# Performance work log

Measured on AMD Instinct MI355X. Metric: run time of the kernel, lower is better.

The kernel has to match this reference:

```python
import jax, jax.numpy as jnp
import numpy as np

FEATURE_DIM = 256
TEMP = 0.1
BASE_TEMP = 0.07
MAX_SAMPLES = 1024
SIM_THR = 0.7


def setup_inputs() -> dict:
    key = jax.random.key(0)
    ks = jax.random.split(key, 8)
    B, C, H, W = 4, FEATURE_DIM, 160, 160
    s = 1.0 / np.sqrt(C)
    return {
        'feats': jax.random.normal(ks[0], (B, C, H, W), jnp.float32),
        'labels': jax.random.randint(ks[1], (B, H, W), 0, 2).astype(jnp.int64),
        'superpixel_indice': jax.random.randint(ks[2], (B, H, W), 0, 200).astype(jnp.int64),
        'w1': jax.random.normal(ks[3], (C, C), jnp.float32) * s,
        'b1': jnp.zeros((C,), jnp.float32),
        'w2': jax.random.normal(ks[4], (C, C), jnp.float32) * s,
        'b2': jnp.zeros((C,), jnp.float32),
        'wa1': jax.random.normal(ks[5], (64, C), jnp.float32) * s,
        'ba1': jnp.zeros((64,), jnp.float32),
        'wa2': jax.random.normal(ks[6], (1, 64), jnp.float32) * (1.0 / 8.0),
        'ba2': jnp.zeros((1,), jnp.float32),
    }


def _per_sample(f, w, lab, sp):
    # f: (N, C) normalized proj feats, w: (N,) pixel weights, lab/sp: (N,) int
    valid = lab == 1
    # deterministic sample: stable-sort valid pixels to the front, take MAX_SAMPLES
    order = jnp.argsort(jnp.where(valid, 0, 1).astype(jnp.int32))
    idx = order[:MAX_SAMPLES]
    sel = valid[idx]                       # (S,) real-sample mask (pads if <S valid)
    tf = f[idx]                            # (S, C)
    tw = w[idx]                            # (S,)
    ts = sp[idx]                           # (S,)
    sim = tf @ tf.T                        # (S, S)
    S = MAX_SAMPLES
    eye = jnp.eye(S, dtype=bool)
    pos = (ts[:, None] == ts[None, :]) & (sim > SIM_THR)
    pos = pos & sel[:, None] & sel[None, :] & ~eye
    exp_sim = jnp.exp(sim / TEMP) * sel[None, :].astype(sim.dtype)
    denom = exp_sim.sum(axis=1)            # (S,)
    log_prob = sim / TEMP - jnp.log(jnp.where(denom > 0, denom, 1.0))[:, None]
    pw = tw[:, None] * tw[None, :]
    pwm = jnp.where(pos, pw, 0.0)
    psum = pwm.sum()
    loss = -(TEMP / BASE_TEMP) * (pwm * jnp.where(pos, log_prob, 0.0)).sum() / jnp.where(psum > 0, psum, 1.0)
    has = psum > 0
    return jnp.where(has, loss, 0.0), has


def reference(feats, labels, superpixel_indice, w1, b1, w2, b2, wa1, ba1, wa2, ba2):
    B, C, H, W = feats.shape
    x = jnp.transpose(feats, (0, 2, 3, 1)).reshape(B, H * W, C)  # (B, N, C)
    proj = jax.nn.relu(x @ w1.T + b1) @ w2.T + b2                # 1x1 convs == per-pixel matmul
    attn = jax.nn.sigmoid(jax.nn.relu(x @ wa1.T + ba1) @ wa2.T + ba2)[..., 0]  # (B, N)
    nrm = jnp.linalg.norm(proj, axis=-1, keepdims=True)
    fn = proj / jnp.maximum(nrm, 1e-12)
    lab = labels.reshape(B, -1)
    sp = superpixel_indice.reshape(B, -1)
    losses, flags = jax.vmap(_per_sample)(fn, attn, lab, sp)
    n = flags.sum().astype(jnp.float32)
    return jnp.where(n > 0, losses.sum() / jnp.maximum(n, 1.0), 0.0)
```

## Files before the change

### kernel.cpp

```cpp
#include <hip/hip_runtime.h>
#include <hip/hip_bf16.h>
#include <math.h>

#define NPIX   25600
#define CDIM   256
#define SSEL   1024
#define BATCH  4
#define NCHUNK 25
#define INV_T  10.0f
#define RATIO  1.4285714285714286f
#define THR    0.7f

typedef __attribute__((ext_vector_type(8))) short bf16x8;
typedef __attribute__((ext_vector_type(4))) float f32x4;
typedef unsigned short u16;

__device__ __forceinline__ void bf16_split(float v, u16& h, u16& l) {
  __hip_bfloat16 hb = __float2bfloat16(v);
  __hip_bfloat16 lb = __float2bfloat16(v - __bfloat162float(hb));
  h = *reinterpret_cast<u16*>(&hb);
  l = *reinterpret_cast<u16*>(&lb);
}

__global__ __launch_bounds__(256) void pack_weights(
    const float* __restrict__ w1, const float* __restrict__ w2,
    const float* __restrict__ wa1, const int* __restrict__ labels,
    u16* __restrict__ w1hb, u16* __restrict__ w1lb,
    u16* __restrict__ w2hb, u16* __restrict__ w2lb,
    u16* __restrict__ wahb, u16* __restrict__ walb,
    float* __restrict__ denom, float* __restrict__ Prow, float* __restrict__ Ssum,
    float* __restrict__ nrm, int* __restrict__ counts) {
  int t = threadIdx.x;
  int e = blockIdx.x * 256 + t;
  if (e < 65536) {
    bf16_split(w1[e], w1hb[e], w1lb[e]);
    bf16_split(w2[e], w2hb[e], w2lb[e]);
  }
  if (e < 16384) bf16_split(wa1[e], wahb[e], walb[e]);
  if (e < BATCH * SSEL) { denom[e] = 0.f; Prow[e] = 0.f; nrm[e] = 0.f; }
  if (e < BATCH) Ssum[e] = 0.f;

  if (blockIdx.x < BATCH * NCHUNK) {
    int b = blockIdx.x / NCHUNK, ch = blockIdx.x % NCHUNK;
    const int* lab = labels + b * NPIX + ch * 1024;
    int local = 0;
#pragma unroll
    for (int qq = 0; qq < 4; ++qq) local += (lab[qq * 256 + t] == 1);
    for (int off = 32; off > 0; off >>= 1) local += __shfl_xor(local, off, 64);
    __shared__ int ws[4];
    if ((t & 63) == 0) ws[t >> 6] = local;
    __syncthreads();
    if (t == 0) counts[blockIdx.x] = ws[0] + ws[1] + ws[2] + ws[3];
  }
}

__global__ __launch_bounds__(1024) void select_scatter(
    const int* __restrict__ labels, const int* __restrict__ sp,
    const int* __restrict__ counts,
    int* __restrict__ idx, int* __restrict__ selv, int* __restrict__ tsp) {
  int b = blockIdx.x / NCHUNK, ch = blockIdx.x % NCHUNK;
  int t = threadIdx.x;
  __shared__ int cs[NCHUNK];
  __shared__ int wave_tot[16];
  if (t < NCHUNK) cs[t] = counts[b * NCHUNK + t];
  __syncthreads();
  int Vtot = 0, vbase = 0;
#pragma unroll
  for (int c = 0; c < NCHUNK; ++c) {
    int v = cs[c];
    Vtot += v;
    if (c < ch) vbase += v;
  }
  int ibase = ch * 1024 - vbase;

  int i = ch * 1024 + t;
  int isv = (labels[b * NPIX + i] == 1) ? 1 : 0;
  int lane = t & 63, wid = t >> 6;
  unsigned long long mv = __ballot(isv);
  int pv = __popcll(mv & ((1ull << lane) - 1ull));
  if (lane == 0) wave_tot[wid] = __popcll(mv);
  __syncthreads();
  for (int w = 0; w < wid; ++w) pv += wave_tot[w];
  int gslot = isv ? (vbase + pv) : (Vtot + ibase + (t - pv));
  if (gslot < SSEL) {
    idx [b * SSEL + gslot] = i;
    selv[b * SSEL + gslot] = isv;
    tsp [b * SSEL + gslot] = sp[b * NPIX + i];
  }
}

__global__ __launch_bounds__(256) void gather_cast(
    const float* __restrict__ feats, const int* __restrict__ idx,
    u16* __restrict__ xh, u16* __restrict__ xl) {
  int r0 = blockIdx.x * 16;
  int b  = r0 >> 10;
  int t  = threadIdx.x;
  __shared__ int ridx[16];
  if (t < 16) ridx[t] = idx[r0 + t];
  __syncthreads();
  const float* fb = feats + ((long)b * CDIM + t) * NPIX;
#pragma unroll 4
  for (int r = 0; r < 16; ++r) {
    float v = fb[ridx[r]];
    u16 h, l;
    bf16_split(v, h, l);
    long o = (long)(r0 + r) * CDIM + t;
    xh[o] = h;
    xl[o] = l;
  }
}

__global__ __launch_bounds__(256) void gemm1_kernel(
    const u16* __restrict__ xh, const u16* __restrict__ xl,
    const u16* __restrict__ w1hb, const u16* __restrict__ w1lb,
    const u16* __restrict__ wahb, const u16* __restrict__ walb,
    const float* __restrict__ b1, const float* __restrict__ ba1,
    const float* __restrict__ wa2, const float* __restrict__ ba2,
    u16* __restrict__ hh, u16* __restrict__ hl, float* __restrict__ tw) {
  int n  = blockIdx.x;
  int i0 = blockIdx.y * 64;
  int t = threadIdx.x;
  int lane = t & 63, w = t >> 6, m = lane & 15, q = lane >> 4;
  bool attn = (n == 4);
  const u16* bsh = attn ? wahb : (w1hb + n * 64 * 256);
  const u16* bsl = attn ? walb : (w1lb + n * 64 * 256);

  __shared__ __align__(16) u16 Ah[64 * 72], Al[64 * 72];
  __shared__ __align__(16) u16 Bh[64 * 72], Bl[64 * 72];

  f32x4 acc[4];
#pragma unroll
  for (int nt = 0; nt < 4; ++nt) acc[nt] = {0.f, 0.f, 0.f, 0.f};

  for (int kk = 0; kk < 4; ++kk) {
    __syncthreads();
#pragma unroll
    for (int p = 0; p < 2; ++p) {
      int e = p * 256 + t;
      int row = e >> 3, kg = e & 7;
      int lo = row * 72 + kg * 8;
      int go = row * 256 + kk * 64 + kg * 8;
      *(uint4*)&Ah[lo] = *(const uint4*)&xh[(i0 + row) * 256 + kk * 64 + kg * 8];
      *(uint4*)&Al[lo] = *(const uint4*)&xl[(i0 + row) * 256 + kk * 64 + kg * 8];
      *(uint4*)&Bh[lo] = *(const uint4*)&bsh[go];
      *(uint4*)&Bl[lo] = *(const uint4*)&bsl[go];
    }
    __syncthreads();
#pragma unroll
    for (int ks = 0; ks < 2; ++ks) {
      int koff = ks * 32 + q * 8;
      bf16x8 ah = *(const bf16x8*)&Ah[(w * 16 + m) * 72 + koff];
      bf16x8 al = *(const bf16x8*)&Al[(w * 16 + m) * 72 + koff];
#pragma unroll
      for (int nt = 0; nt < 4; ++nt) {
        bf16x8 bh = *(const bf16x8*)&Bh[(nt * 16 + m) * 72 + koff];
        bf16x8 bl = *(const bf16x8*)&Bl[(nt * 16 + m) * 72 + koff];
        acc[nt] = __builtin_amdgcn_mfma_f32_16x16x32_bf16(ah, bh, acc[nt], 0, 0, 0);
        acc[nt] = __builtin_amdgcn_mfma_f32_16x16x32_bf16(ah, bl, acc[nt], 0, 0, 0);
        acc[nt] = __builtin_amdgcn_mfma_f32_16x16x32_bf16(al, bh, acc[nt], 0, 0, 0);
      }
    }
  }

  if (!attn) {
#pragma unroll
    for (int nt = 0; nt < 4; ++nt) {
      int col = n * 64 + nt * 16 + m;
      float bb = b1[col];
#pragma unroll
      for (int reg = 0; reg < 4; ++reg) {
        int row = i0 + w * 16 + q * 4 + reg;
        float v = fmaxf(acc[nt][reg] + bb, 0.f);
        u16 h, l;
        bf16_split(v, h, l);
        hh[row * 256 + col] = h;
        hl[row * 256 + col] = l;
      }
    }
  } else {
    float part[4] = {0.f, 0.f, 0.f, 0.f};
#pragma unroll
    for (int nt = 0; nt < 4; ++nt) {
      int ca = nt * 16 + m;
      float bb = ba1[ca], wv = wa2[ca];
#pragma unroll
      for (int reg = 0; reg < 4; ++reg)
        part[reg] += fmaxf(acc[nt][reg] + bb, 0.f) * wv;
    }
    for (int off = 8; off > 0; off >>= 1) {
#pragma unroll
      for (int reg = 0; reg < 4; ++reg)
        part[reg] += __shfl_xor(part[reg], off, 64);
    }
    if (m == 0) {
      float bb2 = ba2[0];
#pragma unroll
      for (int reg = 0; reg < 4; ++reg) {
        int row = i0 + w * 16 + q * 4 + reg;
        tw[row] = 1.f / (1.f + expf(-(part[reg] + bb2)));
      }
    }
  }
}

__global__ __launch_bounds__(256) void gemm2_kernel(
    const u16* __restrict__ hh, const u16* __restrict__ hl,
    const u16* __restrict__ w2hb, const u16* __restrict__ w2lb,
    const float* __restrict__ b2,
    float* __restrict__ pbuf, float* __restrict__ nrm) {
  int n  = blockIdx.x;
  int i0 = blockIdx.y * 64;
  int t = threadIdx.x;
  int lane = t & 63, w = t >> 6, m = lane & 15, q = lane >> 4;
  const u16* bsh = w2hb + n * 64 * 256;
  const u16* bsl = w2lb + n * 64 * 256;

  __shared__ __align__(16) u16 Ah[64 * 72], Al[64 * 72];
  __shared__ __align__(16) u16 Bh[64 * 72], Bl[64 * 72];

  f32x4 acc[4];
#pragma unroll
  for (int nt = 0; nt < 4; ++nt) acc[nt] = {0.f, 0.f, 0.f, 0.f};

  for (int kk = 0; kk < 4; ++kk) {
    __syncthreads();
#pragma unroll
    for (int p = 0; p < 2; ++p) {
      int e = p * 256 + t;
      int row = e >> 3, kg = e & 7;
      int lo = row * 72 + kg * 8;
      int go = row * 256 + kk * 64 + kg * 8;
      *(uint4*)&Ah[lo] = *(const uint4*)&hh[(i0 + row) * 256 + kk * 64 + kg * 8];
      *(uint4*)&Al[lo] = *(const uint4*)&hl[(i0 + row) * 256 + kk * 64 + kg * 8];
      *(uint4*)&Bh[lo] = *(const uint4*)&bsh[go];
      *(uint4*)&Bl[lo] = *(const uint4*)&bsl[go];
    }
    __syncthreads();
#pragma unroll
    for (int ks = 0; ks < 2; ++ks) {
      int koff = ks * 32 + q * 8;
      bf16x8 ah = *(const bf16x8*)&Ah[(w * 16 + m) * 72 + koff];
      bf16x8 al = *(const bf16x8*)&Al[(w * 16 + m) * 72 + koff];
#pragma unroll
      for (int nt = 0; nt < 4; ++nt) {
        bf16x8 bh = *(const bf16x8*)&Bh[(nt * 16 + m) * 72 + koff];
        bf16x8 bl = *(const bf16x8*)&Bl[(nt * 16 + m) * 72 + koff];
        acc[nt] = __builtin_amdgcn_mfma_f32_16x16x32_bf16(ah, bh, acc[nt], 0, 0, 0);
        acc[nt] = __builtin_amdgcn_mfma_f32_16x16x32_bf16(ah, bl, acc[nt], 0, 0, 0);
        acc[nt] = __builtin_amdgcn_mfma_f32_16x16x32_bf16(al, bh, acc[nt], 0, 0, 0);
      }
    }
  }

  float part[4] = {0.f, 0.f, 0.f, 0.f};
#pragma unroll
  for (int nt = 0; nt < 4; ++nt) {
    int col = n * 64 + nt * 16 + m;
    float bb = b2[col];
#pragma unroll
    for (int reg = 0; reg < 4; ++reg) {
      int row = i0 + w * 16 + q * 4 + reg;
      float p = acc[nt][reg] + bb;
      pbuf[row * 256 + col] = p;
      part[reg] += p * p;
    }
  }
  for (int off = 8; off > 0; off >>= 1) {
#pragma unroll
    for (int reg = 0; reg < 4; ++reg)
      part[reg] += __shfl_xor(part[reg], off, 64);
  }
  if (m == 0) {
#pragma unroll
    for (int reg = 0; reg < 4; ++reg) {
      int row = i0 + w * 16 + q * 4 + reg;
      atomicAdd(&nrm[row], part[reg]);
    }
  }
}

__global__ __launch_bounds__(256) void norm_split(
    const float* __restrict__ pbuf, const float* __restrict__ nrm,
    u16* __restrict__ fnh, u16* __restrict__ fnl) {
  int e = blockIdx.x * 256 + threadIdx.x;
  long base = (long)e * 8;
  int row = e >> 5;
  float inv = 1.f / fmaxf(sqrtf(nrm[row]), 1e-12f);
  float4 pa = *(const float4*)&pbuf[base];
  float4 pb = *(const float4*)&pbuf[base + 4];
  float v[8] = {pa.x, pa.y, pa.z, pa.w, pb.x, pb.y, pb.z, pb.w};
  u16 hs[8], ls[8];
#pragma unroll
  for (int j = 0; j < 8; ++j) bf16_split(v[j] * inv, hs[j], ls[j]);
  *(uint4*)&fnh[base] = *(const uint4*)hs;
  *(uint4*)&fnl[base] = *(const uint4*)ls;
}

__global__ __launch_bounds__(256) void sim_kernel(
    const u16* __restrict__ fnh, const u16* __restrict__ fnl,
    const float* __restrict__ tw,
    const int* __restrict__ selv, const int* __restrict__ tsp,
    float* __restrict__ denom, float* __restrict__ Prow, float* __restrict__ Ssum) {
  int b = blockIdx.y;
  int t = threadIdx.x;
  int lane = t & 63, w = t >> 6;
  int m = lane & 15, q = lane >> 4;

  int rem = blockIdx.x, ti = 0;
  while (rem >= (16 - ti)) { rem -= (16 - ti); ++ti; }
  int tj = ti + rem;
  bool diag = (ti == tj);
  int i0 = ti * 64, j0 = tj * 64;
  int base = b << 10;

  __shared__ __align__(16) u16 Ah[64 * 72], Al[64 * 72];
  __shared__ __align__(16) u16 Bhh[64 * 72], Bll[64 * 72];
  __shared__ float drl[64], Prl[64];
  __shared__ float dclw[4][64], Pclw[4][64];
  __shared__ float swv[4];

  const u16* Bh = diag ? Ah : Bhh;
  const u16* Bl = diag ? Al : Bll;

  f32x4 acc[4];
#pragma unroll
  for (int nt = 0; nt < 4; ++nt) acc[nt] = {0.f, 0.f, 0.f, 0.f};

  for (int kk = 0; kk < 4; ++kk) {
    __syncthreads();
#pragma unroll
    for (int p = 0; p < 2; ++p) {
      int e = p * 256 + t;
      int row = e >> 3, kg = e & 7;
      int lo = row * 72 + kg * 8;
      int gi_ = (base + i0 + row) * 256 + kk * 64 + kg * 8;
      *(uint4*)&Ah[lo] = *(const uint4*)&fnh[gi_];
      *(uint4*)&Al[lo] = *(const uint4*)&fnl[gi_];
      if (!diag) {
        int gj_ = (base + j0 + row) * 256 + kk * 64 + kg * 8;
        *(uint4*)&Bhh[lo] = *(const uint4*)&fnh[gj_];
        *(uint4*)&Bll[lo] = *(const uint4*)&fnl[gj_];
      }
    }
    __syncthreads();
#pragma unroll
    for (int ks = 0; ks < 2; ++ks) {
      int koff = ks * 32 + q * 8;
      int arow = w * 16 + m;
      bf16x8 ah = *(const bf16x8*)&Ah[arow * 72 + koff];
      bf16x8 al = *(const bf16x8*)&Al[arow * 72 + koff];
#pragma unroll
      for (int nt = 0; nt < 4; ++nt) {
        bf16x8 bh = *(const bf16x8*)&Bh[(nt * 16 + m) * 72 + koff];
        bf16x8 bl = *(const bf16x8*)&Bl[(nt * 16 + m) * 72 + koff];
        acc[nt] = __builtin_amdgcn_mfma_f32_16x16x32_bf16(ah, bh, acc[nt], 0, 0, 0);
        acc[nt] = __builtin_amdgcn_mfma_f32_16x16x32_bf16(ah, bl, acc[nt], 0, 0, 0);
        acc[nt] = __builtin_amdgcn_mfma_f32_16x16x32_bf16(al, bh, acc[nt], 0, 0, 0);
      }
    }
  }

  int   gi[4], gj[4], si[4], sj[4], ci[4], cj[4];
  float twi[4], twj[4];
#pragma unroll
  for (int reg = 0; reg < 4; ++reg) {
    int i = i0 + w * 16 + q * 4 + reg;
    gi[reg] = i; twi[reg] = tw[base + i];
    si[reg] = selv[base + i]; ci[reg] = tsp[base + i];
  }
#pragma unroll
  for (int nt = 0; nt < 4; ++nt) {
    int j = j0 + nt * 16 + m;
    gj[nt] = j; twj[nt] = tw[base + j];
    sj[nt] = selv[base + j]; cj[nt] = tsp[base + j];
  }

  float dR[4] = {0, 0, 0, 0}, PR[4] = {0, 0, 0, 0};
  float dC[4] = {0, 0, 0, 0}, PC[4] = {0, 0, 0, 0};
  float Sp = 0.f;
#pragma unroll
  for (int nt = 0; nt < 4; ++nt) {
#pragma unroll
    for (int reg = 0; reg < 4; ++reg) {
      float s = acc[nt][reg];
      float e10 = __expf(s * INV_T);
      if (sj[nt]) dR[reg] += e10;
      if (si[reg]) dC[nt] += e10;
      if (si[reg] && sj[nt] && (ci[reg] == cj[nt]) && (s > THR) && (gi[reg] != gj[nt])) {
        float pw = twi[reg] * twj[nt];
        PR[reg] += pw;
        PC[nt] += pw;
        Sp += pw * s;
      }
    }
  }

  for (int off = 8; off > 0; off >>= 1) {
#pragma unroll
    for (int reg = 0; reg < 4; ++reg) {
      dR[reg] += __shfl_xor(dR[reg], off, 64);
      PR[reg] += __shfl_xor(PR[reg], off, 64);
    }
  }
  if (m == 0) {
#pragma unroll
    for (int reg = 0; reg < 4; ++reg) {
      drl[w * 16 + q * 4 + reg] = dR[reg];
      Prl[w * 16 + q * 4 + reg] = PR[reg];
    }
  }
  if (!diag) {
    for (int off = 32; off >= 16; off >>= 1) {
#pragma unroll
      for (int nt = 0; nt < 4; ++nt) {
        dC[nt] += __shfl_xor(dC[nt], off, 64);
        PC[nt] += __shfl_xor(PC[nt], off, 64);
      }
    }
    if (q == 0) {
#pragma unroll
      for (int nt = 0; nt < 4; ++nt) {
        dclw[w][nt * 16 + m] = dC[nt];
        Pclw[w][nt * 16 + m] = PC[nt];
      }
    }
  }
  for (int off = 32; off > 0; off >>= 1) Sp += __shfl_xor(Sp, off, 64);
  if (lane == 0) swv[w] = Sp;
  __syncthreads();

  if (t < 64) {
    atomicAdd(&denom[base + i0 + t], drl[t]);
    atomicAdd(&Prow [base + i0 + t], Prl[t]);
    if (!diag) {
      float dc = dclw[0][t] + dclw[1][t] + dclw[2][t] + dclw[3][t];
      float pc = Pclw[0][t] + Pclw[1][t] + Pclw[2][t] + Pclw[3][t];
      atomicAdd(&denom[base + j0 + t], dc);
      atomicAdd(&Prow [base + j0 + t], pc);
    }
  }
  if (t == 0) {
    float St = swv[0] + swv[1] + swv[2] + swv[3];
    atomicAdd(&Ssum[b], diag ? St : 2.f * St);
  }
}

__global__ __launch_bounds__(1024) void finalize_kernel(
    const float* __restrict__ denom, const float* __restrict__ Prow,
    const float* __restrict__ Ssum, float* __restrict__ out) {
  int t = threadIdx.x;
  int b = t >> 8, u = t & 255;
  float P = 0.f, L = 0.f;
#pragma unroll
  for (int q = 0; q < 4; ++q) {
    int s = u + q * 256;
    float p = Prow[b * SSEL + s];
    float D = denom[b * SSEL + s];
    P += p;
    L += p * logf(D > 0.f ? D : 1.f);
  }
  for (int off = 32; off > 0; off >>= 1) {
    P += __shfl_xor(P, off, 64);
    L += __shfl_xor(L, off, 64);
  }
  __shared__ float wP[16], wL[16];
  int lane = t & 63, w = t >> 6;
  if (lane == 0) { wP[w] = P; wL[w] = L; }
  __syncthreads();
  if (t == 0) {
    float total = 0.f, n = 0.f;
    for (int bb = 0; bb < BATCH; ++bb) {
      float psum = wP[4 * bb] + wP[4 * bb + 1] + wP[4 * bb + 2] + wP[4 * bb + 3];
      float lsum = wL[4 * bb] + wL[4 * bb + 1] + wL[4 * bb + 2] + wL[4 * bb + 3];
      if (psum > 0.f) {
        float wls = Ssum[bb] * INV_T - lsum;
        total += -RATIO * wls / psum;
        n += 1.f;
      }
    }
    out[0] = (n > 0.f) ? (total / n) : 0.f;
  }
}

extern "C" void kernel_launch(void* const* d_in, const int* in_sizes, int n_in,
                              void* d_out, int out_size, void* d_ws, size_t ws_size,
                              hipStream_t stream) {
  const float* feats = (const float*)d_in[0];
  const int*   labels = (const int*)d_in[1];
  const int*   sp     = (const int*)d_in[2];
  const float* w1  = (const float*)d_in[3];
  const float* b1  = (const float*)d_in[4];
  const float* w2  = (const float*)d_in[5];
  const float* b2  = (const float*)d_in[6];
  const float* wa1 = (const float*)d_in[7];
  const float* ba1 = (const float*)d_in[8];
  const float* wa2 = (const float*)d_in[9];
  const float* ba2 = (const float*)d_in[10];
  float* out = (float*)d_out;

  char* W = (char*)d_ws;
  u16* w1hb = (u16*)W;               W += 65536 * 2;
  u16* w1lb = (u16*)W;               W += 65536 * 2;
  u16* w2hb = (u16*)W;               W += 65536 * 2;
  u16* w2lb = (u16*)W;               W += 65536 * 2;
  u16* wahb = (u16*)W;               W += 16384 * 2;
  u16* walb = (u16*)W;               W += 16384 * 2;
  u16* xh   = (u16*)W;               W += 1048576 * 2;
  u16* xl   = (u16*)W;               W += 1048576 * 2;
  u16* hh   = (u16*)W;               W += 1048576 * 2;
  u16* hl   = (u16*)W;               W += 1048576 * 2;
  u16* fnh  = (u16*)W;               W += 1048576 * 2;
  u16* fnl  = (u16*)W;               W += 1048576 * 2;
  float* pbuf = (float*)W;           W += 1048576 * 4;
  float* nrm  = (float*)W;           W += 4096 * 4;
  float* tw   = (float*)W;           W += 4096 * 4;
  float* denom= (float*)W;           W += 4096 * 4;
  float* Prow = (float*)W;           W += 4096 * 4;
  float* Ssum = (float*)W;           W += 4 * 4;
  int*   idx  = (int*)W;             W += 4096 * 4;
  int*   selv = (int*)W;             W += 4096 * 4;
  int*   tsp  = (int*)W;             W += 4096 * 4;
  int*   counts = (int*)W;           W += 128 * 4;

  pack_weights<<<256, 256, 0, stream>>>(w1, w2, wa1, labels,
                                        w1hb, w1lb, w2hb, w2lb, wahb, walb,
                                        denom, Prow, Ssum, nrm, counts);
  select_scatter<<<BATCH * NCHUNK, 1024, 0, stream>>>(labels, sp, counts,
                                                      idx, selv, tsp);
  gather_cast<<<256, 256, 0, stream>>>(feats, idx, xh, xl);
  gemm1_kernel<<<dim3(5, 64), 256, 0, stream>>>(xh, xl, w1hb, w1lb, wahb, walb,
                                                b1, ba1, wa2, ba2, hh, hl, tw);
  gemm2_kernel<<<dim3(4, 64), 256, 0, stream>>>(hh, hl, w2hb, w2lb, b2,
                                                pbuf, nrm);
  norm_split<<<512, 256, 0, stream>>>(pbuf, nrm, fnh, fnl);
  sim_kernel<<<dim3(136, BATCH), 256, 0, stream>>>(fnh, fnl, tw, selv, tsp,
                                                   denom, Prow, Ssum);
  finalize_kernel<<<1, 1024, 0, stream>>>(denom, Prow, Ssum, out);
}
```

Before: 195.8 us.

## Drop split-bf16 emulation for single bf16 MFMA and fuse gemm2 with row normalization

Replaces the hi/lo bf16 split (three MFMAs per product, which emulates near-fp32 accuracy) with plain bf16 operands and a single MFMA in all three GEMMs and the similarity kernel. This halves the intermediate buffers and their memory traffic. It also fuses gemm2 with L2 normalization: each block computes a full 256-column row tile and normalizes it in registers, which removes the pbuf round trip, the atomics and the norm_split kernel. The risk is precision, since similarity values are scaled by 1/T=10 before exp and thresholded at 0.7, so bf16 rounding could change the loss or flip borderline positives. The fused gemm2 also launches only 64 blocks.

```diff
diff --git a/kernel.cpp b/kernel.cpp
--- a/kernel.cpp
+++ b/kernel.cpp
@@ -15,29 +15,25 @@
 typedef __attribute__((ext_vector_type(4))) float f32x4;
 typedef unsigned short u16;
 
-__device__ __forceinline__ void bf16_split(float v, u16& h, u16& l) {
-  __hip_bfloat16 hb = __float2bfloat16(v);
-  __hip_bfloat16 lb = __float2bfloat16(v - __bfloat162float(hb));
-  h = *reinterpret_cast<u16*>(&hb);
-  l = *reinterpret_cast<u16*>(&lb);
+__device__ __forceinline__ u16 to_bf16(float v) {
+  __hip_bfloat16 h = __float2bfloat16(v);
+  return *reinterpret_cast<u16*>(&h);
 }
 
 __global__ __launch_bounds__(256) void pack_weights(
     const float* __restrict__ w1, const float* __restrict__ w2,
     const float* __restrict__ wa1, const int* __restrict__ labels,
-    u16* __restrict__ w1hb, u16* __restrict__ w1lb,
-    u16* __restrict__ w2hb, u16* __restrict__ w2lb,
-    u16* __restrict__ wahb, u16* __restrict__ walb,
+    u16* __restrict__ w1b, u16* __restrict__ w2b, u16* __restrict__ wab,
     float* __restrict__ denom, float* __restrict__ Prow, float* __restrict__ Ssum,
-    float* __restrict__ nrm, int* __restrict__ counts) {
+    int* __restrict__ counts) {
   int t = threadIdx.x;
   int e = blockIdx.x * 256 + t;
   if (e < 65536) {
-    bf16_split(w1[e], w1hb[e], w1lb[e]);
-    bf16_split(w2[e], w2hb[e], w2lb[e]);
-  }
-  if (e < 16384) bf16_split(wa1[e], wahb[e], walb[e]);
-  if (e < BATCH * SSEL) { denom[e] = 0.f; Prow[e] = 0.f; nrm[e] = 0.f; }
+    w1b[e] = to_bf16(w1[e]);
+    w2b[e] = to_bf16(w2[e]);
+  }
+  if (e < 16384) wab[e] = to_bf16(wa1[e]);
+  if (e < BATCH * SSEL) { denom[e] = 0.f; Prow[e] = 0.f; }
   if (e < BATCH) Ssum[e] = 0.f;
 
   if (blockIdx.x < BATCH * NCHUNK) {
@@ -91,7 +87,7 @@
 
 __global__ __launch_bounds__(256) void gather_cast(
     const float* __restrict__ feats, const int* __restrict__ idx,
-    u16* __restrict__ xh, u16* __restrict__ xl) {
+    u16* __restrict__ xh) {
   int r0 = blockIdx.x * 16;
   int b  = r0 >> 10;
   int t  = threadIdx.x;
@@ -101,32 +97,25 @@
   const float* fb = feats + ((long)b * CDIM + t) * NPIX;
 #pragma unroll 4
   for (int r = 0; r < 16; ++r) {
-    float v = fb[ridx[r]];
-    u16 h, l;
-    bf16_split(v, h, l);
-    long o = (long)(r0 + r) * CDIM + t;
-    xh[o] = h;
-    xl[o] = l;
+    xh[(long)(r0 + r) * CDIM + t] = to_bf16(fb[ridx[r]]);
   }
 }
 
 __global__ __launch_bounds__(256) void gemm1_kernel(
-    const u16* __restrict__ xh, const u16* __restrict__ xl,
-    const u16* __restrict__ w1hb, const u16* __restrict__ w1lb,
-    const u16* __restrict__ wahb, const u16* __restrict__ walb,
+    const u16* __restrict__ xh, const u16* __restrict__ w1b,
+    const u16* __restrict__ wab,
     const float* __restrict__ b1, const float* __restrict__ ba1,
     const float* __restrict__ wa2, const float* __restrict__ ba2,
-    u16* __restrict__ hh, u16* __restrict__ hl, float* __restrict__ tw) {
+    u16* __restrict__ hh, float* __restrict__ tw) {
   int n  = blockIdx.x;
   int i0 = blockIdx.y * 64;
   int t = threadIdx.x;
   int lane = t & 63, w = t >> 6, m = lane & 15, q = lane >> 4;
   bool attn = (n == 4);
-  const u16* bsh = attn ? wahb : (w1hb + n * 64 * 256);
-  const u16* bsl = attn ? walb : (w1lb + n * 64 * 256);
-
-  __shared__ __align__(16) u16 Ah[64 * 72], Al[64 * 72];
-  __shared__ __align__(16) u16 Bh[64 * 72], Bl[64 * 72];
+  const u16* bsrc = attn ? wab : (w1b + n * 64 * 256);
+
+  __shared__ __align__(16) u16 Ah[64 * 72];
+  __shared__ __align__(16) u16 Bh[64 * 72];
 
   f32x4 acc[4];
 #pragma unroll
@@ -139,25 +128,18 @@
       int e = p * 256 + t;
       int row = e >> 3, kg = e & 7;
       int lo = row * 72 + kg * 8;
-      int go = row * 256 + kk * 64 + kg * 8;
       *(uint4*)&Ah[lo] = *(const uint4*)&xh[(i0 + row) * 256 + kk * 64 + kg * 8];
-      *(uint4*)&Al[lo] = *(const uint4*)&xl[(i0 + row) * 256 + kk * 64 + kg * 8];
-      *(uint4*)&Bh[lo] = *(const uint4*)&bsh[go];
-      *(uint4*)&Bl[lo] = *(const uint4*)&bsl[go];
+      *(uint4*)&Bh[lo] = *(const uint4*)&bsrc[row * 256 + kk * 64 + kg * 8];
     }
     __syncthreads();
 #pragma unroll
     for (int ks = 0; ks < 2; ++ks) {
       int koff = ks * 32 + q * 8;
       bf16x8 ah = *(const bf16x8*)&Ah[(w * 16 + m) * 72 + koff];
-      bf16x8 al = *(const bf16x8*)&Al[(w * 16 + m) * 72 + koff];
 #pragma unroll
       for (int nt = 0; nt < 4; ++nt) {
         bf16x8 bh = *(const bf16x8*)&Bh[(nt * 16 + m) * 72 + koff];
-        bf16x8 bl = *(const bf16x8*)&Bl[(nt * 16 + m) * 72 + koff];
         acc[nt] = __builtin_amdgcn_mfma_f32_16x16x32_bf16(ah, bh, acc[nt], 0, 0, 0);
-        acc[nt] = __builtin_amdgcn_mfma_f32_16x16x32_bf16(ah, bl, acc[nt], 0, 0, 0);
-        acc[nt] = __builtin_amdgcn_mfma_f32_16x16x32_bf16(al, bh, acc[nt], 0, 0, 0);
       }
     }
   }
@@ -170,11 +152,7 @@
 #pragma unroll
       for (int reg = 0; reg < 4; ++reg) {
         int row = i0 + w * 16 + q * 4 + reg;
-        float v = fmaxf(acc[nt][reg] + bb, 0.f);
-        u16 h, l;
-        bf16_split(v, h, l);
-        hh[row * 256 + col] = h;
-        hl[row * 256 + col] = l;
+        hh[row * 256 + col] = to_bf16(fmaxf(acc[nt][reg] + bb, 0.f));
       }
     }
   } else {
@@ -203,102 +181,83 @@
   }
 }
 
-__global__ __launch_bounds__(256) void gemm2_kernel(
-    const u16* __restrict__ hh, const u16* __restrict__ hl,
-    const u16* __restrict__ w2hb, const u16* __restrict__ w2lb,
-    const float* __restrict__ b2,
-    float* __restrict__ pbuf, float* __restrict__ nrm) {
-  int n  = blockIdx.x;
-  int i0 = blockIdx.y * 64;
+__global__ __launch_bounds__(256) void gemm2norm_kernel(
+    const u16* __restrict__ hh, const u16* __restrict__ w2b,
+    const float* __restrict__ b2, u16* __restrict__ fnb) {
+  int i0 = blockIdx.x * 64;
   int t = threadIdx.x;
   int lane = t & 63, w = t >> 6, m = lane & 15, q = lane >> 4;
-  const u16* bsh = w2hb + n * 64 * 256;
-  const u16* bsl = w2lb + n * 64 * 256;
-
-  __shared__ __align__(16) u16 Ah[64 * 72], Al[64 * 72];
-  __shared__ __align__(16) u16 Bh[64 * 72], Bl[64 * 72];
-
-  f32x4 acc[4];
-#pragma unroll
-  for (int nt = 0; nt < 4; ++nt) acc[nt] = {0.f, 0.f, 0.f, 0.f};
-
-  for (int kk = 0; kk < 4; ++kk) {
-    __syncthreads();
-#pragma unroll
-    for (int p = 0; p < 2; ++p) {
-      int e = p * 256 + t;
-      int row = e >> 3, kg = e & 7;
-      int lo = row * 72 + kg * 8;
-      int go = row * 256 + kk * 64 + kg * 8;
-      *(uint4*)&Ah[lo] = *(const uint4*)&hh[(i0 + row) * 256 + kk * 64 + kg * 8];
-      *(uint4*)&Al[lo] = *(const uint4*)&hl[(i0 + row) * 256 + kk * 64 + kg * 8];
-      *(uint4*)&Bh[lo] = *(const uint4*)&bsh[go];
-      *(uint4*)&Bl[lo] = *(const uint4*)&bsl[go];
-    }
-    __syncthreads();
-#pragma unroll
-    for (int ks = 0; ks < 2; ++ks) {
+
+  __shared__ __align__(16) u16 Bs[64 * 264];
+
+  bf16x8 af[8];
+#pragma unroll
+  for (int ks = 0; ks < 8; ++ks)
+    af[ks] = *(const bf16x8*)&hh[(i0 + w * 16 + m) * 256 + ks * 32 + q * 8];
+
+  f32x4 acc[4][4];
+#pragma unroll
+  for (int n = 0; n < 4; ++n)
+#pragma unroll
+    for (int nt = 0; nt < 4; ++nt) acc[n][nt] = {0.f, 0.f, 0.f, 0.f};
+
+  for (int n = 0; n < 4; ++n) {
+    __syncthreads();
+#pragma unroll
+    for (int i = 0; i < 8; ++i) {
+      int e = i * 256 + t;
+      int row = e >> 5, kg = e & 31;
+      *(uint4*)&Bs[row * 264 + kg * 8] = *(const uint4*)&w2b[(n * 64 + row) * 256 + kg * 8];
+    }
+    __syncthreads();
+#pragma unroll
+    for (int ks = 0; ks < 8; ++ks) {
       int koff = ks * 32 + q * 8;
-      bf16x8 ah = *(const bf16x8*)&Ah[(w * 16 + m) * 72 + koff];
-      bf16x8 al = *(const bf16x8*)&Al[(w * 16 + m) * 72 + koff];
 #pragma unroll
       for (int nt = 0; nt < 4; ++nt) {
-        bf16x8 bh = *(const bf16x8*)&Bh[(nt * 16 + m) * 72 + koff];
-        bf16x8 bl = *(const bf16x8*)&Bl[(nt * 16 + m) * 72 + koff];
-        acc[nt] = __builtin_amdgcn_mfma_f32_16x16x32_bf16(ah, bh, acc[nt], 0, 0, 0);
-        acc[nt] = __builtin_amdgcn_mfma_f32_16x16x32_bf16(ah, bl, acc[nt], 0, 0, 0);
-        acc[nt] = __builtin_amdgcn_mfma_f32_16x16x32_bf16(al, bh, acc[nt], 0, 0, 0);
-      }
-    }
-  }
-
-  float part[4] = {0.f, 0.f, 0.f, 0.f};
-#pragma unroll
-  for (int nt = 0; nt < 4; ++nt) {
-    int col = n * 64 + nt * 16 + m;
-    float bb = b2[col];
-#pragma unroll
-    for (int reg = 0; reg < 4; ++reg) {
-      int row = i0 + w * 16 + q * 4 + reg;
-      float p = acc[nt][reg] + bb;
-      pbuf[row * 256 + col] = p;
-      part[reg] += p * p;
-    }
-  }
+        bf16x8 bh = *(const bf16x8*)&Bs[(nt * 16 + m) * 264 + koff];
+        acc[n][nt] = __builtin_amdgcn_mfma_f32_16x16x32_bf16(af[ks], bh, acc[n][nt], 0, 0, 0);
+      }
+    }
+  }
+
+  float ss[4] = {0.f, 0.f, 0.f, 0.f};
+#pragma unroll
+  for (int n = 0; n < 4; ++n)
+#pragma unroll
+    for (int nt = 0; nt < 4; ++nt) {
+      float bb = b2[n * 64 + nt * 16 + m];
+#pragma unroll
+      for (int reg = 0; reg < 4; ++reg) {
+        float p = acc[n][nt][reg] + bb;
+        acc[n][nt][reg] = p;
+        ss[reg] += p * p;
+      }
+    }
   for (int off = 8; off > 0; off >>= 1) {
 #pragma unroll
-    for (int reg = 0; reg < 4; ++reg)
-      part[reg] += __shfl_xor(part[reg], off, 64);
-  }
-  if (m == 0) {
-#pragma unroll
-    for (int reg = 0; reg < 4; ++reg) {
-      int row = i0 + w * 16 + q * 4 + reg;
-      atomicAdd(&nrm[row], part[reg]);
-    }
-  }
-}
-
-__global__ __launch_bounds__(256) void norm_split(
-    const float* __restrict__ pbuf, const float* __restrict__ nrm,
-    u16* __restrict__ fnh, u16* __restrict__ fnl) {
-  int e = blockIdx.x * 256 + threadIdx.x;
-  long base = (long)e * 8;
-  int row = e >> 5;
-  float inv = 1.f / fmaxf(sqrtf(nrm[row]), 1e-12f);
-  float4 pa = *(const float4*)&pbuf[base];
-  float4 pb = *(const float4*)&pbuf[base + 4];
-  float v[8] = {pa.x, pa.y, pa.z, pa.w, pb.x, pb.y, pb.z, pb.w};
-  u16 hs[8], ls[8];
-#pragma unroll
-  for (int j = 0; j < 8; ++j) bf16_split(v[j] * inv, hs[j], ls[j]);
-  *(uint4*)&fnh[base] = *(const uint4*)hs;
-  *(uint4*)&fnl[base] = *(const uint4*)ls;
+    for (int reg = 0; reg < 4; ++reg) ss[reg] += __shfl_xor(ss[reg], off, 64);
+  }
+  float inv[4];
+#pragma unroll
+  for (int reg = 0; reg < 4; ++reg)
+    inv[reg] = 1.f / fmaxf(sqrtf(ss[reg]), 1e-12f);
+
+#pragma unroll
+  for (int n = 0; n < 4; ++n)
+#pragma unroll
+    for (int nt = 0; nt < 4; ++nt) {
+      int col = n * 64 + nt * 16 + m;
+#pragma unroll
+      for (int reg = 0; reg < 4; ++reg) {
+        int row = i0 + w * 16 + q * 4 + reg;
+        fnb[row * 256 + col] = to_bf16(acc[n][nt][reg] * inv[reg]);
+      }
+    }
 }
 
 __global__ __launch_bounds__(256) void sim_kernel(
-    const u16* __restrict__ fnh, const u16* __restrict__ fnl,
-    const float* __restrict__ tw,
+    const u16* __restrict__ fnb, const float* __restrict__ tw,
     const int* __restrict__ selv, const int* __restrict__ tsp,
     float* __restrict__ denom, float* __restrict__ Prow, float* __restrict__ Ssum) {
   int b = blockIdx.y;
@@ -313,14 +272,13 @@
   int i0 = ti * 64, j0 = tj * 64;
   int base = b << 10;
 
-  __shared__ __align__(16) u16 Ah[64 * 72], Al[64 * 72];
-  __shared__ __align__(16) u16 Bhh[64 * 72], Bll[64 * 72];
+  __shared__ __align__(16) u16 Ah[64 * 72];
+  __shared__ __align__(16) u16 Bhh[64 * 72];
   __shared__ float drl[64], Prl[64];
   __shared__ float dclw[4][64], Pclw[4][64];
   __shared__ float swv[4];
 
   const u16* Bh = diag ? Ah : Bhh;
-  const u16* Bl = diag ? Al : Bll;
 
   f32x4 acc[4];
 #pragma unroll
@@ -333,29 +291,19 @@
       int e = p * 256 + t;
       int row = e >> 3, kg = e & 7;
       int lo = row * 72 + kg * 8;
-      int gi_ = (base + i0 + row) * 256 + kk * 64 + kg * 8;
-      *(uint4*)&Ah[lo] = *(const uint4*)&fnh[gi_];
-      *(uint4*)&Al[lo] = *(const uint4*)&fnl[gi_];
-      if (!diag) {
-        int gj_ = (base + j0 + row) * 256 + kk * 64 + kg * 8;
-        *(uint4*)&Bhh[lo] = *(const uint4*)&fnh[gj_];
-        *(uint4*)&Bll[lo] = *(const uint4*)&fnl[gj_];
-      }
+      *(uint4*)&Ah[lo] = *(const uint4*)&fnb[(base + i0 + row) * 256 + kk * 64 + kg * 8];
+      if (!diag)
+        *(uint4*)&Bhh[lo] = *(const uint4*)&fnb[(base + j0 + row) * 256 + kk * 64 + kg * 8];
     }
     __syncthreads();
 #pragma unroll
     for (int ks = 0; ks < 2; ++ks) {
       int koff = ks * 32 + q * 8;
-      int arow = w * 16 + m;
-      bf16x8 ah = *(const bf16x8*)&Ah[arow * 72 + koff];
-      bf16x8 al = *(const bf16x8*)&Al[arow * 72 + koff];
+      bf16x8 ah = *(const bf16x8*)&Ah[(w * 16 + m) * 72 + koff];
 #pragma unroll
       for (int nt = 0; nt < 4; ++nt) {
         bf16x8 bh = *(const bf16x8*)&Bh[(nt * 16 + m) * 72 + koff];
-        bf16x8 bl = *(const bf16x8*)&Bl[(nt * 16 + m) * 72 + koff];
         acc[nt] = __builtin_amdgcn_mfma_f32_16x16x32_bf16(ah, bh, acc[nt], 0, 0, 0);
-        acc[nt] = __builtin_amdgcn_mfma_f32_16x16x32_bf16(ah, bl, acc[nt], 0, 0, 0);
-        acc[nt] = __builtin_amdgcn_mfma_f32_16x16x32_bf16(al, bh, acc[nt], 0, 0, 0);
       }
     }
   }
@@ -499,41 +447,30 @@
   float* out = (float*)d_out;
 
   char* W = (char*)d_ws;
-  u16* w1hb = (u16*)W;               W += 65536 * 2;
-  u16* w1lb = (u16*)W;               W += 65536 * 2;
-  u16* w2hb = (u16*)W;               W += 65536 * 2;
-  u16* w2lb = (u16*)W;               W += 65536 * 2;
-  u16* wahb = (u16*)W;               W += 16384 * 2;
-  u16* walb = (u16*)W;               W += 16384 * 2;
-  u16* xh   = (u16*)W;               W += 1048576 * 2;
-  u16* xl   = (u16*)W;               W += 1048576 * 2;
-  u16* hh   = (u16*)W;               W += 1048576 * 2;
-  u16* hl   = (u16*)W;               W += 1048576 * 2;
-  u16* fnh  = (u16*)W;               W += 1048576 * 2;
-  u16* fnl  = (u16*)W;               W += 1048576 * 2;
-  float* pbuf = (float*)W;           W += 1048576 * 4;
-  float* nrm  = (float*)W;           W += 4096 * 4;
-  float* tw   = (float*)W;           W += 4096 * 4;
-  float* denom= (float*)W;           W += 4096 * 4;
-  float* Prow = (float*)W;           W += 4096 * 4;
-  float* Ssum = (float*)W;           W += 4 * 4;
-  int*   idx  = (int*)W;             W += 4096 * 4;
-  int*   selv = (int*)W;             W += 4096 * 4;
-  int*   tsp  = (int*)W;             W += 4096 * 4;
-  int*   counts = (int*)W;           W += 128 * 4;
-
-  pack_weights<<<256, 256, 0, stream>>>(w1, w2, wa1, labels,
-                                        w1hb, w1lb, w2hb, w2lb, wahb, walb,
-                                        denom, Prow, Ssum, nrm, counts);
+  u16* w1b = (u16*)W;               W += 65536 * 2;
+  u16* w2b = (u16*)W;               W += 65536 * 2;
+  u16* wab = (u16*)W;               W += 16384 * 2;
+  u16* xh  = (u16*)W;               W += 1048576 * 2;
+  u16* hh  = (u16*)W;               W += 1048576 * 2;
+  u16* fnb = (u16*)W;               W += 1048576 * 2;
+  float* tw   = (float*)W;          W += 4096 * 4;
+  float* denom= (float*)W;          W += 4096 * 4;
+  float* Prow = (float*)W;          W += 4096 * 4;
+  float* Ssum = (float*)W;          W += 4 * 4;
+  int*   idx  = (int*)W;            W += 4096 * 4;
+  int*   selv = (int*)W;            W += 4096 * 4;
+  int*   tsp  = (int*)W;            W += 4096 * 4;
+  int*   counts = (int*)W;          W += 128 * 4;
+
+  pack_weights<<<256, 256, 0, stream>>>(w1, w2, wa1, labels, w1b, w2b, wab,
+                                        denom, Prow, Ssum, counts);
   select_scatter<<<BATCH * NCHUNK, 1024, 0, stream>>>(labels, sp, counts,
                                                       idx, selv, tsp);
-  gather_cast<<<256, 256, 0, stream>>>(feats, idx, xh, xl);
-  gemm1_kernel<<<dim3(5, 64), 256, 0, stream>>>(xh, xl, w1hb, w1lb, wahb, walb,
-                                                b1, ba1, wa2, ba2, hh, hl, tw);
-  gemm2_kernel<<<dim3(4, 64), 256, 0, stream>>>(hh, hl, w2hb, w2lb, b2,
-                                                pbuf, nrm);
-  norm_split<<<512, 256, 0, stream>>>(pbuf, nrm, fnh, fnl);
-  sim_kernel<<<dim3(136, BATCH), 256, 0, stream>>>(fnh, fnl, tw, selv, tsp,
+  gather_cast<<<256, 256, 0, stream>>>(feats, idx, xh);
+  gemm1_kernel<<<dim3(5, 64), 256, 0, stream>>>(xh, w1b, wab, b1, ba1,
+                                                wa2, ba2, hh, tw);
+  gemm2norm_kernel<<<64, 256, 0, stream>>>(hh, w2b, b2, fnb);
+  sim_kernel<<<dim3(136, BATCH), 256, 0, stream>>>(fnb, tw, selv, tsp,
                                                    denom, Prow, Ssum);
   finalize_kernel<<<1, 1024, 0, stream>>>(denom, Prow, Ssum, out);
 }
```

New measurement: 194.9 us. No clear change (-0.5%).
